# Optimization experiments

Measured on AMD Instinct MI355X. Metric: run time of the kernel, lower is better.

## Reference

```python
import jax, jax.numpy as jnp
import numpy as np

N_STEPS = 8  # fixed-step RK4 over t in [0, 1]


def setup_inputs() -> dict:
    key = jax.random.key(0)
    ks = jax.random.split(key, 4)
    B, D, H = 512, 64, 512
    x = jax.random.normal(ks[0], (B, D), jnp.float32)
    # MLP vector field f(t, x): input = concat([x, t]) -> H -> H -> D
    W1 = jax.random.normal(ks[1], (D + 1, H), jnp.float32) / jnp.sqrt(D + 1.0)
    b1 = jnp.zeros((H,), jnp.float32)
    W2 = jax.random.normal(ks[2], (H, H), jnp.float32) / jnp.sqrt(float(H))
    b2 = jnp.zeros((H,), jnp.float32)
    W3 = jax.random.normal(ks[3], (H, D), jnp.float32) / jnp.sqrt(float(H))
    b3 = jnp.zeros((D,), jnp.float32)
    return {"x": x, "W1": W1, "b1": b1, "W2": W2, "b2": b2, "W3": W3, "b3": b3}


def reference(x, W1, b1, W2, b2, W3, b3):
    dt = 1.0 / N_STEPS

    def vf_single(t, xi):
        # xi: [D], t: scalar -> [D]
        h = jnp.concatenate([xi, t[None]])
        h = jnp.tanh(h @ W1 + b1)
        h = jnp.tanh(h @ W2 + b2)
        return h @ W3 + b3

    def aug_dyn(t, xb):
        # dx/dt = f(x, t);  d(log_det)/dt = -trace(df/dx)  (exact divergence)
        f_s = lambda xi: vf_single(t, xi)
        dx = jax.vmap(f_s)(xb)                      # [B, D]
        jac = jax.vmap(jax.jacfwd(f_s))(xb)         # [B, D, D]
        tr = jnp.trace(jac, axis1=-2, axis2=-1)     # [B]
        return dx, -tr

    def step(carry, i):
        xb, ld = carry
        t0 = i.astype(jnp.float32) * dt
        k1x, k1l = aug_dyn(t0, xb)
        k2x, k2l = aug_dyn(t0 + 0.5 * dt, xb + 0.5 * dt * k1x)
        k3x, k3l = aug_dyn(t0 + 0.5 * dt, xb + 0.5 * dt * k2x)
        k4x, k4l = aug_dyn(t0 + dt, xb + dt * k3x)
        xb = xb + (dt / 6.0) * (k1x + 2.0 * k2x + 2.0 * k3x + k4x)
        ld = ld + (dt / 6.0) * (k1l + 2.0 * k2l + 2.0 * k3l + k4l)
        return (xb, ld), None

    ld0 = jnp.zeros((x.shape[0],), x.dtype)
    (z, log_det), _ = jax.lax.scan(step, (x, ld0), jnp.arange(N_STEPS))
    return z, log_det
```

## Files before the change

kernel.cpp:

```cpp
#include <hip/hip_runtime.h>

#define NSTEPS 8
#define DT (1.0f / NSTEPS)

typedef __bf16 bfv8 __attribute__((ext_vector_type(8)));
typedef float f32x4 __attribute__((ext_vector_type(4)));

__device__ __forceinline__ float fast_tanh(float x) {
  float e = __expf(2.f * x);
  return 1.f - 2.f * __builtin_amdgcn_rcpf(e + 1.f);
}

__global__ __launch_bounds__(256) void pre_kernel(
    const float* __restrict__ W1, const float* __restrict__ W2,
    const float* __restrict__ W3, __bf16* __restrict__ GtT,
    __bf16* __restrict__ W2T, __bf16* __restrict__ W1T,
    __bf16* __restrict__ W3T) {
  int gid = blockIdx.x * 256 + threadIdx.x;
  if (gid < 262144) {
    int j = gid >> 9, k = gid & 511;
    float s = 0.f;
#pragma unroll
    for (int m = 0; m < 64; ++m)
      s = fmaf(W1[m * 512 + j], W3[k * 64 + m], s);
    GtT[gid] = (__bf16)(s * W2[j * 512 + k]);
  } else if (gid < 524288) {
    int g = gid - 262144;
    int k = g >> 9, j = g & 511;
    W2T[g] = (__bf16)W2[j * 512 + k];
  } else if (gid < 557056) {
    int g = gid - 524288;
    int j = g >> 6, i = g & 63;
    W1T[g] = (__bf16)W1[i * 512 + j];
  } else if (gid < 589824) {
    int g = gid - 557056;
    int m = g >> 9, k = g & 511;
    W3T[g] = (__bf16)W3[k * 64 + m];
  }
}

__global__ __launch_bounds__(512, 2) void cnf_kernel(
    const float* __restrict__ x, const float* __restrict__ W1,
    const float* __restrict__ b1, const float* __restrict__ b2,
    const float* __restrict__ b3, const __bf16* __restrict__ GtT,
    const __bf16* __restrict__ W2T, const __bf16* __restrict__ W1T,
    const __bf16* __restrict__ W3T, float* __restrict__ out) {
  __shared__ __bf16 h1s[16 * 512];
  __shared__ __bf16 h2s[16 * 512];
  __shared__ __bf16 vs[16 * 512];
  __shared__ __bf16 xins[16 * 64];
  __shared__ float xbs[16 * 64];
  __shared__ float kcur[16 * 64];
  __shared__ float kacc[16 * 64];
  __shared__ float trbuf[16];
  __shared__ float ldv[16];
  __shared__ float ldacc[16];

  const int tid = threadIdx.x;
  const int lane = tid & 63;
  const int w = tid >> 6;
  const int lr = lane & 15;
  const int lq = lane >> 4;
  const int rowbase = blockIdx.x * 16;

  for (int e = tid; e < 1024; e += 512) {
    float xv = x[(rowbase + (e >> 6)) * 64 + (e & 63)];
    xbs[e] = xv;
    kacc[e] = 0.f;
    xins[e] = (__bf16)xv;
  }
  if (tid < 16) { trbuf[tid] = 0.f; ldv[tid] = 0.f; ldacc[tid] = 0.f; }
  __syncthreads();

  for (int ev = 0; ev < 4 * NSTEPS; ++ev) {
    const int s = ev >> 2, g = ev & 3;
    const float t = s * DT + ((g == 0) ? 0.f : (g == 3) ? DT : 0.5f * DT);

    {
      bfv8 a0 = *(const bfv8*)&xins[lr * 64 + lq * 8];
      bfv8 a1 = *(const bfv8*)&xins[lr * 64 + 32 + lq * 8];
#pragma unroll
      for (int n = 0; n < 4; ++n) {
        const int col = (w * 4 + n) * 16 + lr;
        const float cinit = b1[col] + t * W1[64 * 512 + col];
        f32x4 C = {cinit, cinit, cinit, cinit};
        const __bf16* brow = W1T + col * 64 + lq * 8;
        C = __builtin_amdgcn_mfma_f32_16x16x32_bf16(a0, *(const bfv8*)brow, C, 0, 0, 0);
        C = __builtin_amdgcn_mfma_f32_16x16x32_bf16(a1, *(const bfv8*)(brow + 32), C, 0, 0, 0);
#pragma unroll
        for (int r = 0; r < 4; ++r) {
          const int row = lq * 4 + r;
          const int boff = row * 1024 + ((col * 2) ^ ((row & 7) << 4));
          *(__bf16*)((char*)h1s + boff) = (__bf16)fast_tanh(C[r]);
        }
      }
    }
    __syncthreads();

    bfv8 A[16];
    {
#pragma unroll
      for (int c = 0; c < 16; ++c) {
        const int boff = lr * 1024 + ((c * 64 + lq * 16) ^ ((lr & 7) << 4));
        A[c] = *(const bfv8*)((char*)h1s + boff);
      }
#pragma unroll
      for (int n = 0; n < 4; ++n) {
        const int col = (w * 4 + n) * 16 + lr;
        const float cinit = b2[col];
        f32x4 C = {cinit, cinit, cinit, cinit};
        const __bf16* brow = W2T + col * 512 + lq * 8;
#pragma unroll
        for (int c = 0; c < 16; ++c)
          C = __builtin_amdgcn_mfma_f32_16x16x32_bf16(
              A[c], *(const bfv8*)(brow + c * 32), C, 0, 0, 0);
#pragma unroll
        for (int r = 0; r < 4; ++r) {
          const int row = lq * 4 + r;
          const float tv = fast_tanh(C[r]);
          const int boff = row * 1024 + ((col * 2) ^ ((row & 7) << 4));
          *(__bf16*)((char*)h2s + boff) = (__bf16)tv;
          *(__bf16*)((char*)vs + boff) = (__bf16)(1.f - tv * tv);
        }
      }
    }
    __syncthreads();

    {
#pragma unroll
      for (int c = 0; c < 16; ++c) {
        const int boff = lr * 1024 + ((c * 64 + lq * 16) ^ ((lr & 7) << 4));
        A[c] = *(const bfv8*)((char*)vs + boff);
      }
      float p[4] = {0.f, 0.f, 0.f, 0.f};
#pragma unroll
      for (int n = 0; n < 4; ++n) {
        const int col = (w * 4 + n) * 16 + lr;
        f32x4 C = {0.f, 0.f, 0.f, 0.f};
        const __bf16* brow = GtT + col * 512 + lq * 8;
#pragma unroll
        for (int c = 0; c < 16; ++c)
          C = __builtin_amdgcn_mfma_f32_16x16x32_bf16(
              A[c], *(const bfv8*)(brow + c * 32), C, 0, 0, 0);
#pragma unroll
        for (int r = 0; r < 4; ++r) {
          const int row = lq * 4 + r;
          const int boff = row * 1024 + ((col * 2) ^ ((row & 7) << 4));
          const float h1v = (float)*(const __bf16*)((char*)h1s + boff);
          p[r] += C[r] * (1.f - h1v * h1v);
        }
      }
#pragma unroll
      for (int r = 0; r < 4; ++r) {
        p[r] += __shfl_xor(p[r], 1);
        p[r] += __shfl_xor(p[r], 2);
        p[r] += __shfl_xor(p[r], 4);
        p[r] += __shfl_xor(p[r], 8);
      }
      if (lr == 0) {
#pragma unroll
        for (int r = 0; r < 4; ++r) atomicAdd(&trbuf[lq * 4 + r], p[r]);
      }
    }

    if (w < 4) {
#pragma unroll
      for (int c = 0; c < 16; ++c) {
        const int boff = lr * 1024 + ((c * 64 + lq * 16) ^ ((lr & 7) << 4));
        A[c] = *(const bfv8*)((char*)h2s + boff);
      }
      const int col = w * 16 + lr;
      const float cinit = b3[col];
      f32x4 C = {cinit, cinit, cinit, cinit};
      const __bf16* brow = W3T + col * 512 + lq * 8;
#pragma unroll
      for (int c = 0; c < 16; ++c)
        C = __builtin_amdgcn_mfma_f32_16x16x32_bf16(
            A[c], *(const bfv8*)(brow + c * 32), C, 0, 0, 0);
#pragma unroll
      for (int r = 0; r < 4; ++r) kcur[(lq * 4 + r) * 64 + col] = C[r];
    }
    __syncthreads();

    {
      const float cnext = (g == 2) ? DT : 0.5f * DT;
      const float wg = (g == 0) ? 1.f : 2.f;
      for (int e = tid; e < 1024; e += 512) {
        const float kv = kcur[e];
        if (g < 3) {
          kacc[e] += wg * kv;
          xins[e] = (__bf16)(xbs[e] + cnext * kv);
        } else {
          const float xn = xbs[e] + (DT / 6.f) * (kacc[e] + kv);
          xbs[e] = xn;
          kacc[e] = 0.f;
          xins[e] = (__bf16)xn;
        }
      }
      if (tid < 16) {
        const float tv = trbuf[tid];
        trbuf[tid] = 0.f;
        if (g < 3) {
          ldacc[tid] += wg * tv;
        } else {
          ldv[tid] -= (DT / 6.f) * (ldacc[tid] + tv);
          ldacc[tid] = 0.f;
        }
      }
    }
    __syncthreads();
  }

  for (int e = tid; e < 1024; e += 512)
    out[(rowbase + (e >> 6)) * 64 + (e & 63)] = xbs[e];
  if (tid < 16) out[512 * 64 + rowbase + tid] = ldv[tid];
}

extern "C" void kernel_launch(void* const* d_in, const int* in_sizes, int n_in,
                              void* d_out, int out_size, void* d_ws,
                              size_t ws_size, hipStream_t stream) {
  const float* x = (const float*)d_in[0];
  const float* W1 = (const float*)d_in[1];
  const float* b1 = (const float*)d_in[2];
  const float* W2 = (const float*)d_in[3];
  const float* b2 = (const float*)d_in[4];
  const float* W3 = (const float*)d_in[5];
  const float* b3 = (const float*)d_in[6];
  float* out = (float*)d_out;
  char* ws = (char*)d_ws;

  __bf16* GtT = (__bf16*)(ws);
  __bf16* W2T = (__bf16*)(ws + (512 << 10));
  __bf16* W1T = (__bf16*)(ws + (1024 << 10));
  __bf16* W3T = (__bf16*)(ws + (1088 << 10));

  pre_kernel<<<2304, 256, 0, stream>>>(W1, W2, W3, GtT, W2T, W1T, W3T);
  cnf_kernel<<<32, 512, 0, stream>>>(x, W1, b1, b2, b3, GtT, W2T, W1T, W3T,
                                     out);
}
```

Measured before the change: 952.5 us.

## Repack weights into MFMA-friendly layout, prefetch B fragments, merge trace and output GEMMs

Weights are repacked in the preprocessing kernel into a k-chunk-major layout so each lane's B fragment load is a contiguous 16-byte access. The layer-2 GEMM now software-pipelines its weight loads through a rotating register buffer with two accumulators, and the trace and W3 GEMMs are merged into one work list split evenly across all 8 waves, with double-buffered prefetch and atomic reduction into shared memory. RK4 state (x, k accumulators, log-det) moves into registers, which removes the separate update phase and one barrier per stage. The cost is higher register pressure and extra LDS atomics for the W3 partial sums.

```diff
diff --git a/kernel.cpp b/kernel.cpp
--- a/kernel.cpp
+++ b/kernel.cpp
@@ -11,50 +11,85 @@
   return 1.f - 2.f * __builtin_amdgcn_rcpf(e + 1.f);
 }
 
+__device__ __forceinline__ f32x4 splat4(float v) {
+  f32x4 r; r[0] = v; r[1] = v; r[2] = v; r[3] = v; return r;
+}
+
 __global__ __launch_bounds__(256) void pre_kernel(
     const float* __restrict__ W1, const float* __restrict__ W2,
-    const float* __restrict__ W3, __bf16* __restrict__ GtT,
-    __bf16* __restrict__ W2T, __bf16* __restrict__ W1T,
-    __bf16* __restrict__ W3T) {
-  int gid = blockIdx.x * 256 + threadIdx.x;
-  if (gid < 262144) {
-    int j = gid >> 9, k = gid & 511;
-    float s = 0.f;
-#pragma unroll
-    for (int m = 0; m < 64; ++m)
-      s = fmaf(W1[m * 512 + j], W3[k * 64 + m], s);
-    GtT[gid] = (__bf16)(s * W2[j * 512 + k]);
-  } else if (gid < 524288) {
-    int g = gid - 262144;
-    int k = g >> 9, j = g & 511;
-    W2T[g] = (__bf16)W2[j * 512 + k];
-  } else if (gid < 557056) {
-    int g = gid - 524288;
-    int j = g >> 6, i = g & 63;
-    W1T[g] = (__bf16)W1[i * 512 + j];
-  } else if (gid < 589824) {
-    int g = gid - 557056;
-    int m = g >> 9, k = g & 511;
-    W3T[g] = (__bf16)W3[k * 64 + m];
+    const float* __restrict__ W3, __bf16* __restrict__ W1P,
+    __bf16* __restrict__ W2P, __bf16* __restrict__ GtP,
+    __bf16* __restrict__ W3P) {
+  int t = blockIdx.x * 256 + threadIdx.x;
+  if (t < 4096) {
+    int kq = t >> 9, col = t & 511;
+    bfv8 o;
+#pragma unroll
+    for (int e = 0; e < 8; ++e) o[e] = (__bf16)W1[(kq * 8 + e) * 512 + col];
+    *(bfv8*)(W1P + t * 8) = o;
+  } else if (t < 36864) {
+    int g = t - 4096;
+    int kc = g >> 9, col = g & 511;
+    bfv8 o;
+#pragma unroll
+    for (int e = 0; e < 8; ++e) o[e] = (__bf16)W2[(kc * 8 + e) * 512 + col];
+    *(bfv8*)(W2P + g * 8) = o;
+  } else if (t < 69632) {
+    int g = t - 36864;
+    int kc = g >> 9, j = g & 511;
+    float w1c[64];
+#pragma unroll
+    for (int m = 0; m < 64; ++m) w1c[m] = W1[m * 512 + j];
+    bfv8 o;
+#pragma unroll
+    for (int e = 0; e < 8; ++e) {
+      int k = kc * 8 + e;
+      float s = 0.f;
+#pragma unroll
+      for (int m = 0; m < 64; ++m) s = fmaf(w1c[m], W3[k * 64 + m], s);
+      o[e] = (__bf16)(s * W2[j * 512 + k]);
+    }
+    *(bfv8*)(GtP + g * 8) = o;
+  } else if (t < 73728) {
+    int g = t - 69632;
+    int kc = g >> 6, m = g & 63;
+    bfv8 o;
+#pragma unroll
+    for (int e = 0; e < 8; ++e) o[e] = (__bf16)W3[(kc * 8 + e) * 64 + m];
+    *(bfv8*)(W3P + g * 8) = o;
+  }
+}
+
+__device__ __forceinline__ void pref_chunk(
+    int id, int lr, int lq, const __bf16* __restrict__ GtP,
+    const __bf16* __restrict__ W3P, const char* vs_c, const char* h2_c,
+    bfv8 (&Ae)[8], bfv8 (&Be)[8]) {
+  const bool isTR = id < 64;
+  const int tl = (isTR ? id : id - 64) >> 1;
+  const int hf = id & 1;
+  const char* ab = isTR ? vs_c : h2_c;
+  const __bf16* bb = isTR ? GtP : W3P;
+  const int ks = isTR ? 4096 : 512;
+  const __bf16* bp = bb + lq * ks + (tl * 16 + lr) * 8 + hf * 32 * ks;
+#pragma unroll
+  for (int c = 0; c < 8; ++c) {
+    Be[c] = *(const bfv8*)(bp + c * 4 * ks);
+    Ae[c] = *(const bfv8*)(ab + lr * 1024 +
+                           ((((hf * 8 + c) * 64) + lq * 16) ^ ((lr & 7) << 4)));
   }
 }
 
 __global__ __launch_bounds__(512, 2) void cnf_kernel(
     const float* __restrict__ x, const float* __restrict__ W1,
     const float* __restrict__ b1, const float* __restrict__ b2,
-    const float* __restrict__ b3, const __bf16* __restrict__ GtT,
-    const __bf16* __restrict__ W2T, const __bf16* __restrict__ W1T,
-    const __bf16* __restrict__ W3T, float* __restrict__ out) {
+    const float* __restrict__ b3, const __bf16* __restrict__ W1P,
+    const __bf16* __restrict__ W2P, const __bf16* __restrict__ GtP,
+    const __bf16* __restrict__ W3P, float* __restrict__ out) {
   __shared__ __bf16 h1s[16 * 512];
   __shared__ __bf16 h2s[16 * 512];
   __shared__ __bf16 vs[16 * 512];
-  __shared__ __bf16 xins[16 * 64];
-  __shared__ float xbs[16 * 64];
   __shared__ float kcur[16 * 64];
-  __shared__ float kacc[16 * 64];
   __shared__ float trbuf[16];
-  __shared__ float ldv[16];
-  __shared__ float ldacc[16];
 
   const int tid = threadIdx.x;
   const int lane = tid & 63;
@@ -62,158 +97,178 @@
   const int lr = lane & 15;
   const int lq = lane >> 4;
   const int rowbase = blockIdx.x * 16;
-
-  for (int e = tid; e < 1024; e += 512) {
-    float xv = x[(rowbase + (e >> 6)) * 64 + (e & 63)];
-    xbs[e] = xv;
-    kacc[e] = 0.f;
-    xins[e] = (__bf16)xv;
-  }
-  if (tid < 16) { trbuf[tid] = 0.f; ldv[tid] = 0.f; ldacc[tid] = 0.f; }
-  __syncthreads();
-
-  for (int ev = 0; ev < 4 * NSTEPS; ++ev) {
-    const int s = ev >> 2, g = ev & 3;
-    const float t = s * DT + ((g == 0) ? 0.f : (g == 3) ? DT : 0.5f * DT);
-
+  const char* h1c = (const char*)h1s;
+  const char* h2c = (const char*)h2s;
+  const char* vsc = (const char*)vs;
+
+  float b1c[4], w1tc[4], b2c[4], b3c[4];
+#pragma unroll
+  for (int n = 0; n < 4; ++n) {
+    const int col = w * 64 + n * 16 + lr;
+    b1c[n] = b1[col];
+    w1tc[n] = W1[64 * 512 + col];
+    b2c[n] = b2[col];
+    b3c[n] = b3[n * 16 + lr];
+  }
+
+  float xb0[8], xb1[8], ka0[8], ka1[8];
+  {
+    const float* xr = x + (rowbase + lr) * 64 + lq * 8;
+#pragma unroll
+    for (int e = 0; e < 8; ++e) {
+      xb0[e] = xr[e]; xb1[e] = xr[32 + e]; ka0[e] = 0.f; ka1[e] = 0.f;
+    }
+  }
+  float ldv = 0.f, ldacc = 0.f;
+
+#pragma unroll 1
+  for (int ev = 0; ev <= 4 * NSTEPS; ++ev) {
+    const int g = ev & 3;
+    bfv8 a0, a1;
+    if (ev == 0) {
+#pragma unroll
+      for (int e = 0; e < 8; ++e) { a0[e] = (__bf16)xb0[e]; a1[e] = (__bf16)xb1[e]; }
+      if (w == 7 && lq == 0) trbuf[lr] = 0.f;
+    } else {
+      const int gp = (ev - 1) & 3;
+      f32x4 q0 = *(const f32x4*)&kcur[lr * 64 + lq * 8];
+      f32x4 q1 = *(const f32x4*)&kcur[lr * 64 + lq * 8 + 4];
+      f32x4 q2 = *(const f32x4*)&kcur[lr * 64 + 32 + lq * 8];
+      f32x4 q3 = *(const f32x4*)&kcur[lr * 64 + 32 + lq * 8 + 4];
+      float kc0[8], kc1[8];
+#pragma unroll
+      for (int e = 0; e < 4; ++e) { kc0[e] = q0[e]; kc0[e + 4] = q1[e]; kc1[e] = q2[e]; kc1[e + 4] = q3[e]; }
+      if (gp < 3) {
+        const float wg = (gp == 0) ? 1.f : 2.f;
+        const float cn = (gp == 2) ? DT : 0.5f * DT;
+#pragma unroll
+        for (int e = 0; e < 8; ++e) {
+          ka0[e] += wg * kc0[e]; ka1[e] += wg * kc1[e];
+          a0[e] = (__bf16)(xb0[e] + cn * kc0[e]);
+          a1[e] = (__bf16)(xb1[e] + cn * kc1[e]);
+        }
+      } else {
+#pragma unroll
+        for (int e = 0; e < 8; ++e) {
+          xb0[e] += (DT / 6.f) * (ka0[e] + kc0[e]);
+          xb1[e] += (DT / 6.f) * (ka1[e] + kc1[e]);
+          ka0[e] = 0.f; ka1[e] = 0.f;
+          a0[e] = (__bf16)xb0[e]; a1[e] = (__bf16)xb1[e];
+        }
+      }
+      if (w == 7 && lq == 0) {
+        const float tv = trbuf[lr];
+        trbuf[lr] = 0.f;
+        if (gp < 3) ldacc += ((gp == 0) ? 1.f : 2.f) * tv;
+        else { ldv -= (DT / 6.f) * (ldacc + tv); ldacc = 0.f; }
+      }
+    }
+    if (ev == 4 * NSTEPS) break;
+
+    const float t = (ev >> 2) * DT + ((g == 0) ? 0.f : (g == 3) ? DT : 0.5f * DT);
+#pragma unroll
+    for (int n = 0; n < 4; ++n) {
+      const int col = w * 64 + n * 16 + lr;
+      bfv8 B0 = *(const bfv8*)(W1P + lq * 4096 + col * 8);
+      bfv8 B1 = *(const bfv8*)(W1P + (lq + 4) * 4096 + col * 8);
+      f32x4 C = splat4(b1c[n] + t * w1tc[n]);
+      C = __builtin_amdgcn_mfma_f32_16x16x32_bf16(a0, B0, C, 0, 0, 0);
+      C = __builtin_amdgcn_mfma_f32_16x16x32_bf16(a1, B1, C, 0, 0, 0);
+#pragma unroll
+      for (int r = 0; r < 4; ++r) {
+        const int row = lq * 4 + r;
+        *(__bf16*)((char*)h1s + row * 1024 + ((col * 2) ^ ((row & 7) << 4))) =
+            (__bf16)fast_tanh(C[r]);
+      }
+    }
+    __syncthreads();
+
+    kcur[tid] = 0.f;
+    kcur[tid + 512] = 0.f;
     {
-      bfv8 a0 = *(const bfv8*)&xins[lr * 64 + lq * 8];
-      bfv8 a1 = *(const bfv8*)&xins[lr * 64 + 32 + lq * 8];
-#pragma unroll
-      for (int n = 0; n < 4; ++n) {
-        const int col = (w * 4 + n) * 16 + lr;
-        const float cinit = b1[col] + t * W1[64 * 512 + col];
-        f32x4 C = {cinit, cinit, cinit, cinit};
-        const __bf16* brow = W1T + col * 64 + lq * 8;
-        C = __builtin_amdgcn_mfma_f32_16x16x32_bf16(a0, *(const bfv8*)brow, C, 0, 0, 0);
-        C = __builtin_amdgcn_mfma_f32_16x16x32_bf16(a1, *(const bfv8*)(brow + 32), C, 0, 0, 0);
-#pragma unroll
-        for (int r = 0; r < 4; ++r) {
-          const int row = lq * 4 + r;
-          const int boff = row * 1024 + ((col * 2) ^ ((row & 7) << 4));
-          *(__bf16*)((char*)h1s + boff) = (__bf16)fast_tanh(C[r]);
+      const __bf16* wbase = W2P + lq * 4096 + (w * 64 + lr) * 8;
+      bfv8 Bb[8];
+#pragma unroll
+      for (int u = 0; u < 8; ++u)
+        Bb[u] = *(const bfv8*)(wbase + (u & 15) * 16384 + (u >> 4) * 128);
+      bfv8 A[16];
+#pragma unroll
+      for (int c = 0; c < 16; ++c)
+        A[c] = *(const bfv8*)(h1c + lr * 1024 +
+                              (((c * 64) + lq * 16) ^ ((lr & 7) << 4)));
+      f32x4 Ca = splat4(0.f), Cb = splat4(0.f);
+#pragma unroll
+      for (int u = 0; u < 64; ++u) {
+        const int c = u & 15, n = u >> 4;
+        if (c == 0) { Ca = splat4(0.f); Cb = splat4(0.f); }
+        if (u & 1)
+          Cb = __builtin_amdgcn_mfma_f32_16x16x32_bf16(A[c], Bb[u & 7], Cb, 0, 0, 0);
+        else
+          Ca = __builtin_amdgcn_mfma_f32_16x16x32_bf16(A[c], Bb[u & 7], Ca, 0, 0, 0);
+        if (u + 8 < 64)
+          Bb[u & 7] = *(const bfv8*)(wbase + ((u + 8) & 15) * 16384 +
+                                     ((u + 8) >> 4) * 128);
+        if (c == 15) {
+#pragma unroll
+          for (int r = 0; r < 4; ++r) {
+            const int row = lq * 4 + r;
+            const int col = w * 64 + n * 16 + lr;
+            const float tv = fast_tanh(Ca[r] + Cb[r] + b2c[n]);
+            const int boff = row * 1024 + ((col * 2) ^ ((row & 7) << 4));
+            *(__bf16*)((char*)h2s + boff) = (__bf16)tv;
+            *(__bf16*)((char*)vs + boff) = (__bf16)(1.f - tv * tv);
+          }
         }
       }
     }
     __syncthreads();
 
-    bfv8 A[16];
     {
-#pragma unroll
-      for (int c = 0; c < 16; ++c) {
-        const int boff = lr * 1024 + ((c * 64 + lq * 16) ^ ((lr & 7) << 4));
-        A[c] = *(const bfv8*)((char*)h1s + boff);
-      }
-#pragma unroll
-      for (int n = 0; n < 4; ++n) {
-        const int col = (w * 4 + n) * 16 + lr;
-        const float cinit = b2[col];
-        f32x4 C = {cinit, cinit, cinit, cinit};
-        const __bf16* brow = W2T + col * 512 + lq * 8;
-#pragma unroll
-        for (int c = 0; c < 16; ++c)
-          C = __builtin_amdgcn_mfma_f32_16x16x32_bf16(
-              A[c], *(const bfv8*)(brow + c * 32), C, 0, 0, 0);
-#pragma unroll
-        for (int r = 0; r < 4; ++r) {
-          const int row = lq * 4 + r;
-          const float tv = fast_tanh(C[r]);
-          const int boff = row * 1024 + ((col * 2) ^ ((row & 7) << 4));
-          *(__bf16*)((char*)h2s + boff) = (__bf16)tv;
-          *(__bf16*)((char*)vs + boff) = (__bf16)(1.f - tv * tv);
+      bfv8 Ab[2][8], Bc[2][8];
+      pref_chunk(w * 9, lr, lq, GtP, W3P, vsc, h2c, Ab[0], Bc[0]);
+#pragma unroll
+      for (int i = 0; i < 9; ++i) {
+        const int id = w * 9 + i;
+        const bool isTR = id < 64;
+        const int tl = (isTR ? id : id - 64) >> 1;
+        if (i < 8)
+          pref_chunk(id + 1, lr, lq, GtP, W3P, vsc, h2c, Ab[(i + 1) & 1],
+                     Bc[(i + 1) & 1]);
+        f32x4 C = splat4((!isTR && (id & 1) == 0) ? b3c[tl] : 0.f);
+#pragma unroll
+        for (int c = 0; c < 8; ++c)
+          C = __builtin_amdgcn_mfma_f32_16x16x32_bf16(Ab[i & 1][c], Bc[i & 1][c],
+                                                      C, 0, 0, 0);
+        if (isTR) {
+#pragma unroll
+          for (int r = 0; r < 4; ++r) {
+            const int row = lq * 4 + r;
+            const int col = tl * 16 + lr;
+            const float h1v = (float)*(const __bf16*)(
+                h1c + row * 1024 + ((col * 2) ^ ((row & 7) << 4)));
+            float p = C[r] * (1.f - h1v * h1v);
+            p += __shfl_xor(p, 1);
+            p += __shfl_xor(p, 2);
+            p += __shfl_xor(p, 4);
+            p += __shfl_xor(p, 8);
+            if (lr == 0) atomicAdd(&trbuf[row], p);
+          }
+        } else {
+#pragma unroll
+          for (int r = 0; r < 4; ++r)
+            atomicAdd(&kcur[(lq * 4 + r) * 64 + tl * 16 + lr], C[r]);
         }
       }
     }
     __syncthreads();
-
-    {
-#pragma unroll
-      for (int c = 0; c < 16; ++c) {
-        const int boff = lr * 1024 + ((c * 64 + lq * 16) ^ ((lr & 7) << 4));
-        A[c] = *(const bfv8*)((char*)vs + boff);
-      }
-      float p[4] = {0.f, 0.f, 0.f, 0.f};
-#pragma unroll
-      for (int n = 0; n < 4; ++n) {
-        const int col = (w * 4 + n) * 16 + lr;
-        f32x4 C = {0.f, 0.f, 0.f, 0.f};
-        const __bf16* brow = GtT + col * 512 + lq * 8;
-#pragma unroll
-        for (int c = 0; c < 16; ++c)
-          C = __builtin_amdgcn_mfma_f32_16x16x32_bf16(
-              A[c], *(const bfv8*)(brow + c * 32), C, 0, 0, 0);
-#pragma unroll
-        for (int r = 0; r < 4; ++r) {
-          const int row = lq * 4 + r;
-          const int boff = row * 1024 + ((col * 2) ^ ((row & 7) << 4));
-          const float h1v = (float)*(const __bf16*)((char*)h1s + boff);
-          p[r] += C[r] * (1.f - h1v * h1v);
-        }
-      }
-#pragma unroll
-      for (int r = 0; r < 4; ++r) {
-        p[r] += __shfl_xor(p[r], 1);
-        p[r] += __shfl_xor(p[r], 2);
-        p[r] += __shfl_xor(p[r], 4);
-        p[r] += __shfl_xor(p[r], 8);
-      }
-      if (lr == 0) {
-#pragma unroll
-        for (int r = 0; r < 4; ++r) atomicAdd(&trbuf[lq * 4 + r], p[r]);
-      }
-    }
-
-    if (w < 4) {
-#pragma unroll
-      for (int c = 0; c < 16; ++c) {
-        const int boff = lr * 1024 + ((c * 64 + lq * 16) ^ ((lr & 7) << 4));
-        A[c] = *(const bfv8*)((char*)h2s + boff);
-      }
-      const int col = w * 16 + lr;
-      const float cinit = b3[col];
-      f32x4 C = {cinit, cinit, cinit, cinit};
-      const __bf16* brow = W3T + col * 512 + lq * 8;
-#pragma unroll
-      for (int c = 0; c < 16; ++c)
-        C = __builtin_amdgcn_mfma_f32_16x16x32_bf16(
-            A[c], *(const bfv8*)(brow + c * 32), C, 0, 0, 0);
-#pragma unroll
-      for (int r = 0; r < 4; ++r) kcur[(lq * 4 + r) * 64 + col] = C[r];
-    }
-    __syncthreads();
-
-    {
-      const float cnext = (g == 2) ? DT : 0.5f * DT;
-      const float wg = (g == 0) ? 1.f : 2.f;
-      for (int e = tid; e < 1024; e += 512) {
-        const float kv = kcur[e];
-        if (g < 3) {
-          kacc[e] += wg * kv;
-          xins[e] = (__bf16)(xbs[e] + cnext * kv);
-        } else {
-          const float xn = xbs[e] + (DT / 6.f) * (kacc[e] + kv);
-          xbs[e] = xn;
-          kacc[e] = 0.f;
-          xins[e] = (__bf16)xn;
-        }
-      }
-      if (tid < 16) {
-        const float tv = trbuf[tid];
-        trbuf[tid] = 0.f;
-        if (g < 3) {
-          ldacc[tid] += wg * tv;
-        } else {
-          ldv[tid] -= (DT / 6.f) * (ldacc[tid] + tv);
-          ldacc[tid] = 0.f;
-        }
-      }
-    }
-    __syncthreads();
-  }
-
-  for (int e = tid; e < 1024; e += 512)
-    out[(rowbase + (e >> 6)) * 64 + (e & 63)] = xbs[e];
-  if (tid < 16) out[512 * 64 + rowbase + tid] = ldv[tid];
+  }
+
+  if (w == 0) {
+    float* orow = out + (rowbase + lr) * 64 + lq * 8;
+#pragma unroll
+    for (int e = 0; e < 8; ++e) { orow[e] = xb0[e]; orow[32 + e] = xb1[e]; }
+  }
+  if (w == 7 && lq == 0) out[512 * 64 + rowbase + lr] = ldv;
 }
 
 extern "C" void kernel_launch(void* const* d_in, const int* in_sizes, int n_in,
@@ -227,14 +282,14 @@
   const float* W3 = (const float*)d_in[5];
   const float* b3 = (const float*)d_in[6];
   float* out = (float*)d_out;
-  char* ws = (char*)d_ws;
-
-  __bf16* GtT = (__bf16*)(ws);
-  __bf16* W2T = (__bf16*)(ws + (512 << 10));
-  __bf16* W1T = (__bf16*)(ws + (1024 << 10));
-  __bf16* W3T = (__bf16*)(ws + (1088 << 10));
-
-  pre_kernel<<<2304, 256, 0, stream>>>(W1, W2, W3, GtT, W2T, W1T, W3T);
-  cnf_kernel<<<32, 512, 0, stream>>>(x, W1, b1, b2, b3, GtT, W2T, W1T, W3T,
+  __bf16* wsb = (__bf16*)d_ws;
+
+  __bf16* W1P = wsb;
+  __bf16* W2P = wsb + 32768;
+  __bf16* GtP = wsb + 294912;
+  __bf16* W3P = wsb + 557056;
+
+  pre_kernel<<<288, 256, 0, stream>>>(W1, W2, W3, W1P, W2P, GtP, W3P);
+  cnf_kernel<<<32, 512, 0, stream>>>(x, W1, b1, b2, b3, W1P, W2P, GtP, W3P,
                                      out);
 }
```

After: 2.052 ms. +115.4%, slower.
